# Kernel optimization log

Measured on AMD Instinct MI355X. Metric: run time of the kernel, lower is better.

## Reference

```python
import jax, jax.numpy as jnp
import numpy as np

N, T = 64, 256
V, E, K = 32000, 256, 128


def setup_inputs() -> dict:
    key = jax.random.key(0)
    ks = jax.random.split(key, 7)
    x = jax.random.randint(ks[0], (N, T), 0, V)
    embed_w = jax.random.normal(ks[1], (V, E), dtype=jnp.float32) * 0.02
    # nn.Linear(embed_dim, K*K, bias=False), weight.uniform_(-1, 1)
    trans_w = jax.random.uniform(ks[2], (K * K, E), dtype=jnp.float32, minval=-1.0, maxval=1.0)
    # nn.Linear(1, K): weight [K,1], bias [K]
    start_w = jax.random.normal(ks[3], (K, 1), dtype=jnp.float32)
    start_b = jax.random.normal(ks[4], (K,), dtype=jnp.float32) * 0.1
    # nn.Embedding(K, K) cluster embeddings
    emb_cluster_w = jax.random.normal(ks[5], (K, K), dtype=jnp.float32)
    # nn.Linear(K, vocab, bias=False), weight.uniform_(-1, 1) -> weight [V, K]
    emit_w = jax.random.uniform(ks[6], (V, K), dtype=jnp.float32, minval=-1.0, maxval=1.0)
    return {"x": x, "embed_w": embed_w, "trans_w": trans_w, "start_w": start_w,
            "start_b": start_b, "emb_cluster_w": emb_cluster_w, "emit_w": emit_w}


def reference(x, embed_w, trans_w, start_w, start_b, emb_cluster_w, emit_w):
    n, t = x.shape
    k = emb_cluster_w.shape[0]
    ex = embed_w[x]                                            # [N,T,E]
    # Emissions: log_softmax(emit(emb_cluster(i))) per cluster -> [K,V]
    log_emit = jax.nn.log_softmax(emb_cluster_w @ emit_w.T, axis=-1)
    log_emit_t = log_emit.T                                    # [V,K]
    # start(dummy): ones[N,1] @ W.T + b = W[:,0]+b, same per row
    pre = jax.nn.log_softmax(start_w[:, 0] + start_b)          # [K]
    pre = jnp.broadcast_to(pre, (n, k))
    xs = (jnp.swapaxes(ex[:, :-1, :], 0, 1),                   # [T-1,N,E]
          x[:, 1:].T)                                          # [T-1,N]
    def step(pre_alpha, inp):
        x_prev, w_t = inp
        tran = jax.nn.log_softmax((x_prev @ trans_w.T).reshape(n, k, k), axis=-1)
        cur = jax.nn.logsumexp(pre_alpha[:, :, None] + tran, axis=1)   # [N,K]
        cur = cur + log_emit_t[w_t]                            # add log p(w_t | state)
        return cur, None
    cur, _ = jax.lax.scan(step, pre, xs)
    return -jnp.mean(jax.nn.logsumexp(cur, axis=1))
```

## Files before the change

### kernel.cpp

```cpp
#include <hip/hip_runtime.h>
#include <cstdint>
#include <cstddef>

#define N_SEQ 64
#define T_LEN 256
#define VOCAB 32000
#define EDIM  256
#define KS    128
#define KK    16384
#define MROWS 16384
#define MREAL 16320
#define GPART 32

typedef short  short8  __attribute__((ext_vector_type(8)));
typedef float  floatx4 __attribute__((ext_vector_type(4)));
typedef int    intx8   __attribute__((ext_vector_type(8)));

#define LGKM_BARRIER() asm volatile("s_waitcnt lgkmcnt(0)\n\ts_barrier" ::: "memory")
#define LGKM_WAIT()    asm volatile("s_waitcnt lgkmcnt(0)" ::: "memory")
#define SBAR() do { asm volatile("s_waitcnt lgkmcnt(0)" ::: "memory"); \
                    __builtin_amdgcn_s_barrier(); \
                    __builtin_amdgcn_sched_barrier(0); } while (0)

static __device__ __forceinline__ unsigned short f2bf(float f) {
  unsigned u = __float_as_uint(f);
  u += 0x7fffu + ((u >> 16) & 1u);
  return (unsigned short)(u >> 16);
}

static __device__ __forceinline__ float bf2f(unsigned short h) {
  return __uint_as_float(((unsigned)h) << 16);
}

static __device__ __forceinline__ float fast_rcp(float x) {
#if __has_builtin(__builtin_amdgcn_rcpf)
  return __builtin_amdgcn_rcpf(x);
#else
  return 1.0f / x;
#endif
}

static __device__ __forceinline__ void gl_lds16(const void* gptr, void* lptr) {
  __builtin_amdgcn_global_load_lds(
      (const __attribute__((address_space(1))) void*)gptr,
      (__attribute__((address_space(3))) void*)lptr, 16, 0, 0);
}

__global__ __launch_bounds__(128) void k_prep(const float* sw, const float* sb, float* pre0) {
  __shared__ float vals[KS];
  __shared__ float MM, LS;
  int tid = threadIdx.x;
  float v = sw[tid] + sb[tid];
  vals[tid] = v;
  __syncthreads();
  if (tid == 0) { float m = vals[0]; for (int i = 1; i < KS; ++i) m = fmaxf(m, vals[i]); MM = m; }
  __syncthreads();
  float e = __expf(v - MM);
  vals[tid] = e;
  __syncthreads();
  if (tid == 0) { float s = 0.f; for (int i = 0; i < KS; ++i) s += vals[i]; LS = MM + __logf(s); }
  __syncthreads();
  pre0[tid] = v - LS;
}

__global__ __launch_bounds__(256) void k_transcvt(const float* tw, unsigned short* tb) {
  int idx = blockIdx.x * 256 + threadIdx.x;
  if (idx >= (KK * EDIM) / 4) return;
  int row = idx >> 6, e4 = idx & 63;
  int rowp = ((row & 127) << 7) | (row >> 7);
  int e4s = (e4 & 0x31) | (((((e4 >> 1) & 7) ^ (rowp & 7))) << 1);
  float4 v = *(const float4*)&tw[(size_t)idx * 4];
  unsigned h0 = f2bf(v.x), h1 = f2bf(v.y), h2 = f2bf(v.z), h3 = f2bf(v.w);
  uint2 o; o.x = h0 | (h1 << 16); o.y = h2 | (h3 << 16);
  *(uint2*)&tb[(size_t)rowp * EDIM + e4s * 4] = o;
}

__global__ __launch_bounds__(256) void k_embed(const int* x, const float* ew, unsigned short* exb) {
  int m = blockIdx.x, e = threadIdx.x;
  int t = m >> 6, n = m & 63;
  float v = 0.f;
  if (m < MREAL) { int tok = x[n * T_LEN + t]; v = ew[(size_t)tok * EDIM + e]; }
  int es = (e & 0xC7) | ((((e >> 3) & 7) ^ (m & 7)) << 3);
  exb[(size_t)m * EDIM + es] = f2bf(v);
}

__global__ __launch_bounds__(256) void k_emitlogits(const float* ecl, const float* emw, float* C) {
  int v0 = blockIdx.x * 64, k0 = blockIdx.y * 64;
  int tid = threadIdx.x;
  __shared__ alignas(16) float At[64 * 17];
  __shared__ alignas(16) float Bt[64 * 17];
  int tx = tid & 15, ty = tid >> 4;
  int r = tid >> 2, q = tid & 3;
  float acc[4][4] = {};
  for (int d0 = 0; d0 < KS; d0 += 16) {
    float4 av = *(const float4*)&ecl[(size_t)(k0 + r) * KS + d0 + q * 4];
    float4 bv = *(const float4*)&emw[(size_t)(v0 + r) * KS + d0 + q * 4];
    __syncthreads();
    At[r * 17 + q * 4 + 0] = av.x; At[r * 17 + q * 4 + 1] = av.y;
    At[r * 17 + q * 4 + 2] = av.z; At[r * 17 + q * 4 + 3] = av.w;
    Bt[r * 17 + q * 4 + 0] = bv.x; Bt[r * 17 + q * 4 + 1] = bv.y;
    Bt[r * 17 + q * 4 + 2] = bv.z; Bt[r * 17 + q * 4 + 3] = bv.w;
    __syncthreads();
    #pragma unroll
    for (int dd = 0; dd < 16; ++dd) {
      float a[4], b[4];
      #pragma unroll
      for (int i = 0; i < 4; ++i) a[i] = At[(ty * 4 + i) * 17 + dd];
      #pragma unroll
      for (int i = 0; i < 4; ++i) b[i] = Bt[(tx * 4 + i) * 17 + dd];
      #pragma unroll
      for (int i = 0; i < 4; ++i)
        #pragma unroll
        for (int jj = 0; jj < 4; ++jj) acc[i][jj] += a[i] * b[jj];
    }
  }
  #pragma unroll
  for (int i = 0; i < 4; ++i) {
    float4 o; o.x = acc[i][0]; o.y = acc[i][1]; o.z = acc[i][2]; o.w = acc[i][3];
    *(float4*)&C[(size_t)(k0 + ty * 4 + i) * VOCAB + v0 + tx * 4] = o;
  }
}

__global__ __launch_bounds__(256) void k_lsec(const float* C, float* lseC) {
  int k = blockIdx.x, tid = threadIdx.x;
  __shared__ float sm[4], ss[4];
  const float* row = C + (size_t)k * VOCAB;
  float m = -1e30f;
  for (int v = tid; v < VOCAB; v += 256) m = fmaxf(m, row[v]);
  #pragma unroll
  for (int s = 1; s < 64; s <<= 1) m = fmaxf(m, __shfl_xor(m, s));
  if ((tid & 63) == 0) sm[tid >> 6] = m;
  __syncthreads();
  m = fmaxf(fmaxf(sm[0], sm[1]), fmaxf(sm[2], sm[3]));
  float sum = 0.f;
  for (int v = tid; v < VOCAB; v += 256) sum += __expf(row[v] - m);
  #pragma unroll
  for (int s = 1; s < 64; s <<= 1) sum += __shfl_xor(sum, s);
  if ((tid & 63) == 0) ss[tid >> 6] = sum;
  __syncthreads();
  if (tid == 0) lseC[k] = m + __logf(ss[0] + ss[1] + ss[2] + ss[3]);
}

__global__ __launch_bounds__(128) void k_emis(const int* x, const float* C, const float* lseC,
                                              float* emis, float* emax) {
  int t = blockIdx.x + 1;
  int n = blockIdx.y;
  int k = threadIdx.x;
  __shared__ float red[2];
  int w = x[n * T_LEN + t];
  float v = C[(size_t)k * VOCAB + w] - lseC[k];
  emis[(size_t)((n << 8) + t) * KS + k] = v;
  float m = v;
  #pragma unroll
  for (int s = 1; s < 64; s <<= 1) m = fmaxf(m, __shfl_xor(m, s));
  if ((k & 63) == 0) red[k >> 6] = m;
  __syncthreads();
  if (k == 0) emax[n * T_LEN + t] = fmaxf(red[0], red[1]);
}

__global__ __launch_bounds__(256) void k_comb(const unsigned short* srowPh, float* srowR, float* wcomb,
                                              const float* emis, const float* emax,
                                              int m_base, int Rcap, int rows) {
  int id = blockIdx.x * 256 + threadIdx.x;
  if (id >= rows * KS) return;
  float s = 0.f;
  #pragma unroll
  for (int g = 0; g < GPART; ++g) s += bf2f(srowPh[(size_t)g * Rcap * KS + id]);
  float r = 1.0f / s;
  srowR[(size_t)m_base * KS + id] = r;
  int m = m_base + (id >> 7);
  int t = m >> 6, n = m & 63, k = id & 127;
  float wv = 0.f;
  if (t >= 1) {
    float e  = emis[(size_t)((n << 8) + t) * KS + k];
    float ex = emax[n * T_LEN + t];
    wv = __expf(e - ex) * r * 4096.0f;
  }
  wcomb[(size_t)m_base * KS + id] = wv;
}

static __device__ __forceinline__ void load_S2(const unsigned char* Sbase, int j, int kg, intx8& sf) {
  const uint4* p = (const uint4*)(Sbase + (size_t)j * 128 + kg * 32);
  uint4 a = p[0], b = p[1];
  sf[0] = a.x; sf[1] = a.y; sf[2] = a.z; sf[3] = a.w;
  sf[4] = b.x; sf[5] = b.y; sf[6] = b.z; sf[7] = b.w;
}

static __device__ __forceinline__ void scan_step4(
    int i, int L, int t, int t0s, int tLast, int n, int tid, int kg, int j0, int j1,
    const unsigned char* Ss, const float* wcomb, const float* emis, const float* emax,
    unsigned char* uL8, float* c0sh,
    intx8& uf, intx8& s0, intx8& s1, float& w0, float& w1, float& ex,
    float& M, float& pre_0, float& pre_1) {
  const float LNS = 8.317766167f;
  floatx4 cz = {0.f, 0.f, 0.f, 0.f};
  floatx4 d0 = __builtin_amdgcn_mfma_scale_f32_16x16x128_f8f6f4(
      uf, s0, cz, 0, 0, 0, 0x7F7F7F7F, 0, 0x7F7F7F7F);
  floatx4 d1 = __builtin_amdgcn_mfma_scale_f32_16x16x128_f8f6f4(
      uf, s1, cz, 0, 0, 0, 0x7F7F7F7F, 0, 0x7F7F7F7F);
  float cv0 = d0[0], cv1 = d1[0];
  int tp = t + 2; if (tp > tLast) tp = tLast;
  const unsigned char* Sp = Ss + (size_t)((tp - t0s) * 64 + n) * KK;
  load_S2(Sp, j0, kg, s0);
  load_S2(Sp, j1, kg, s1);
  if (tid == 0) *c0sh = cv0;
  SBAR();
  if (i < L - 1) {
    float c0 = *c0sh;
    float rc = fast_rcp(c0);
    float u0 = cv0 * w0 * rc, u1 = cv1 * w1 * rc;
    int pk0 = __builtin_amdgcn_cvt_pk_fp8_f32(u0, u0, 0, 0);
    int pk1 = __builtin_amdgcn_cvt_pk_fp8_f32(u1, u1, 0, 0);
    if (kg == 0) {
      uL8[j0] = (unsigned char)(pk0 & 0xff);
      uL8[j1] = (unsigned char)(pk1 & 0xff);
    }
    M += ex + __logf(c0) - LNS;
    w0 = wcomb[(size_t)(tp * 64 + n) * KS + j0];
    w1 = wcomb[(size_t)(tp * 64 + n) * KS + j1];
    ex = emax[n * T_LEN + tp];
    SBAR();
    uint4 ua = *(const uint4*)&uL8[kg * 32];
    uint4 ub = *(const uint4*)&uL8[kg * 32 + 16];
    uf[0] = ua.x; uf[1] = ua.y; uf[2] = ua.z; uf[3] = ua.w;
    uf[4] = ub.x; uf[5] = ub.y; uf[6] = ub.z; uf[7] = ub.w;
  } else {
    float em0 = emis[(size_t)((n << 8) + tLast) * KS + j0];
    float em1 = emis[(size_t)((n << 8) + tLast) * KS + j1];
    pre_0 = M - LNS + __logf(cv0) + em0;
    pre_1 = M - LNS + __logf(cv1) + em1;
    SBAR();
  }
}

__global__ __launch_bounds__(256, 2) void k_fused(
    const unsigned short* exb, const unsigned short* trb,
    unsigned char* Sg, unsigned short* srowPh, int m_base, int Rcap,
    const unsigned char* Ss, const float* srowR, const float* wcomb,
    const float* emis, const float* emax, const float* pre0,
    float* alphaG, float* nll, int t0s, int tcs) {
  __shared__ alignas(16) unsigned short As[128 * 64];
  __shared__ alignas(16) unsigned short Bs[128 * 64];
  __shared__ alignas(16) unsigned char uL8[KS];
  __shared__ float c0sh;
  __shared__ float redW[4], redE[4];

  if (blockIdx.x < 64) {
    if (tcs <= 0) return;
    int n = blockIdx.x;
    int tid = threadIdx.x;
    int w = tid >> 6, ln = tid & 63;
    int l15 = ln & 15, kg = ln >> 4;
    int q0 = w * 2;
    int j0 = q0 * 16 + l15, j1 = j0 + 16;
    const float SCALE = 4096.0f;
    int L = tcs, t1 = t0s + tcs, tLast = t1 - 1;
    const float* a0 = (t0s == 1) ? pre0 : (alphaG + (size_t)n * KS);
    float pre_0 = a0[j0], pre_1 = a0[j1];
    float lm = fmaxf(pre_0, pre_1);
    #pragma unroll
    for (int s2 = 1; s2 < 16; s2 <<= 1) lm = fmaxf(lm, __shfl_xor(lm, s2));
    if (ln == 0) redW[w] = lm;
    SBAR();
    float M = fmaxf(fmaxf(redW[0], redW[1]), fmaxf(redW[2], redW[3]));
    {
      float r0 = srowR[(size_t)((t0s - 1) * 64 + n) * KS + j0];
      float r1 = srowR[(size_t)((t0s - 1) * 64 + n) * KS + j1];
      float u0 = __expf(pre_0 - M) * r0 * SCALE;
      float u1 = __expf(pre_1 - M) * r1 * SCALE;
      int pk0 = __builtin_amdgcn_cvt_pk_fp8_f32(u0, u0, 0, 0);
      int pk1 = __builtin_amdgcn_cvt_pk_fp8_f32(u1, u1, 0, 0);
      if (kg == 0) {
        uL8[j0] = (unsigned char)(pk0 & 0xff);
        uL8[j1] = (unsigned char)(pk1 & 0xff);
      }
    }
    SBAR();
    intx8 uf;
    {
      uint4 ua = *(const uint4*)&uL8[kg * 32];
      uint4 ub = *(const uint4*)&uL8[kg * 32 + 16];
      uf[0] = ua.x; uf[1] = ua.y; uf[2] = ua.z; uf[3] = ua.w;
      uf[4] = ub.x; uf[5] = ub.y; uf[6] = ub.z; uf[7] = ub.w;
    }
    intx8 sA0, sA1, sB0, sB1;
    load_S2(Ss + (size_t)n * KK, j0, kg, sA0);
    load_S2(Ss + (size_t)n * KK, j1, kg, sA1);
    int iB = (L > 1) ? 1 : 0;
    const unsigned char* SpB = Ss + (size_t)(iB * 64 + n) * KK;
    load_S2(SpB, j0, kg, sB0);
    load_S2(SpB, j1, kg, sB1);
    int tB = t0s + iB;
    float wA0 = wcomb[(size_t)(t0s * 64 + n) * KS + j0];
    float wA1 = wcomb[(size_t)(t0s * 64 + n) * KS + j1];
    float wB0 = wcomb[(size_t)(tB * 64 + n) * KS + j0];
    float wB1 = wcomb[(size_t)(tB * 64 + n) * KS + j1];
    float exA = emax[n * T_LEN + t0s];
    float exB = emax[n * T_LEN + tB];
    int i = 0, t = t0s;
    for (;;) {
      scan_step4(i, L, t, t0s, tLast, n, tid, kg, j0, j1, Ss, wcomb, emis, emax,
                 uL8, &c0sh, uf, sA0, sA1, wA0, wA1, exA, M, pre_0, pre_1);
      if (++i >= L) break; ++t;
      scan_step4(i, L, t, t0s, tLast, n, tid, kg, j0, j1, Ss, wcomb, emis, emax,
                 uL8, &c0sh, uf, sB0, sB1, wB0, wB1, exB, M, pre_0, pre_1);
      if (++i >= L) break; ++t;
    }
    if (kg == 0) {
      alphaG[(size_t)n * KS + j0] = pre_0;
      alphaG[(size_t)n * KS + j1] = pre_1;
    }
    if (t1 == T_LEN) {
      float m2 = fmaxf(pre_0, pre_1);
      #pragma unroll
      for (int s2 = 1; s2 < 16; s2 <<= 1) m2 = fmaxf(m2, __shfl_xor(m2, s2));
      if (ln == 0) redW[w] = m2;
      SBAR();
      m2 = fmaxf(fmaxf(redW[0], redW[1]), fmaxf(redW[2], redW[3]));
      float le = __expf(pre_0 - m2) + __expf(pre_1 - m2);
      #pragma unroll
      for (int s2 = 1; s2 < 16; s2 <<= 1) le += __shfl_xor(le, s2);
      if (ln == 0) redE[w] = le;
      SBAR();
      if (tid == 0) nll[n] = m2 + __logf(redE[0] + redE[1] + redE[2] + redE[3]);
    }
    return;
  }

  int g = blockIdx.x - 64;
  int bx = g >> 5, grp = g & 31;
  int tid = threadIdx.x, wv = tid >> 6, ln = tid & 63;
  int wc = wv & 1, wm = wv >> 1;
  int m0 = m_base + bx * 128;
  int lr = ln & 15, lk = (ln >> 4) * 8;
  int lg = ln >> 4;
  floatx4 sacc[4][4] = {};
  for (int byi = 0; byi < 4; ++byi) {
    int by = grp * 4 + byi;
    int c0 = by * 128;
    floatx4 acc[4][4] = {};
    for (int k0 = 0; k0 < EDIM; k0 += 64) {
      #pragma unroll
      for (int r = 0; r < 4; ++r) {
        int chunk = (wv * 4 + r) * 64 + ln;
        int row = chunk >> 3, c8 = chunk & 7;
        gl_lds16(&exb[(size_t)(m0 + row) * EDIM + k0 + c8 * 8], &As[(wv * 4 + r) * 512]);
        gl_lds16(&trb[(size_t)(c0 + row) * EDIM + k0 + c8 * 8], &Bs[(wv * 4 + r) * 512]);
      }
      __syncthreads();
      #pragma unroll
      for (int kk = 0; kk < 64; kk += 32) {
        int sw = ((((kk + lk) >> 3) ^ (lr & 7)) << 3);
        short8 af[4], bf[4];
        #pragma unroll
        for (int f = 0; f < 4; ++f)
          af[f] = *(const short8*)&As[(wm * 64 + f * 16 + lr) * 64 + sw];
        #pragma unroll
        for (int f = 0; f < 4; ++f)
          bf[f] = *(const short8*)&Bs[(wc * 64 + f * 16 + lr) * 64 + sw];
        #pragma unroll
        for (int fc = 0; fc < 4; ++fc)
          #pragma unroll
          for (int fm = 0; fm < 4; ++fm)
            acc[fc][fm] = __builtin_amdgcn_mfma_f32_16x16x32_bf16(bf[fc], af[fm], acc[fc][fm], 0, 0, 0);
      }
      LGKM_BARRIER();
    }
    unsigned char* Ts = (unsigned char*)As;
    #pragma unroll
    for (int fc = 0; fc < 4; ++fc) {
      #pragma unroll
      for (int fm = 0; fm < 4; ++fm) {
        floatx4 a = acc[fc][fm];
        float e0 = __expf(a[0]), e1 = __expf(a[1]), e2 = __expf(a[2]), e3 = __expf(a[3]);
        int pq = __builtin_amdgcn_cvt_pk_fp8_f32(e0, e1, 0, 0);
        pq = __builtin_amdgcn_cvt_pk_fp8_f32(e2, e3, pq, 1);
        int mloc = wm * 64 + fm * 16 + lr;
        int cl = wc * 64 + fc * 16 + lg * 4;
        *(int*)&Ts[mloc * 128 + (cl ^ ((mloc & 7) << 4))] = pq;
        sacc[fc][fm][0] += e0; sacc[fc][fm][1] += e1;
        sacc[fc][fm][2] += e2; sacc[fc][fm][3] += e3;
      }
    }
    LGKM_BARRIER();
    #pragma unroll
    for (int r = 0; r < 4; ++r) {
      int seg = r * 256 + tid;
      int mloc = seg >> 3, s = seg & 7;
      uint4 v = *(const uint4*)&Ts[mloc * 128 + ((s ^ (mloc & 7)) << 4)];
      *(uint4*)&Sg[(size_t)(bx * 128 + mloc) * KK + c0 + s * 16] = v;
    }
    LGKM_BARRIER();
  }
  #pragma unroll
  for (int fc = 0; fc < 4; ++fc) {
    #pragma unroll
    for (int fm = 0; fm < 4; ++fm) {
      int mloc = bx * 128 + wm * 64 + fm * 16 + lr;
      int i = wc * 64 + fc * 16 + lg * 4;
      ushort4 h;
      h.x = f2bf(sacc[fc][fm][0]); h.y = f2bf(sacc[fc][fm][1]);
      h.z = f2bf(sacc[fc][fm][2]); h.w = f2bf(sacc[fc][fm][3]);
      *(ushort4*)&srowPh[((size_t)grp * Rcap + mloc) * KS + i] = h;
    }
  }
}

__global__ __launch_bounds__(64) void k_final(const float* nll, float* out) {
  int tid = threadIdx.x;
  float v = nll[tid];
  #pragma unroll
  for (int s = 1; s < 64; s <<= 1) v += __shfl_xor(v, s);
  if (tid == 0) out[0] = -v / 64.0f;
}

extern "C" void kernel_launch(void* const* d_in, const int* in_sizes, int n_in,
                              void* d_out, int out_size, void* d_ws, size_t ws_size,
                              hipStream_t stream) {
  const int*   x       = (const int*)d_in[0];
  const float* embed_w = (const float*)d_in[1];
  const float* trans_w = (const float*)d_in[2];
  const float* start_w = (const float*)d_in[3];
  const float* start_b = (const float*)d_in[4];
  const float* ecl     = (const float*)d_in[5];
  const float* emw     = (const float*)d_in[6];

  char* w = (char*)d_ws;
  size_t off = 0;
  auto alloc = [&](size_t bytes) -> char* {
    char* p = w + off;
    off = (off + bytes + 255) & ~(size_t)255;
    return p;
  };
  float*          pre0   = (float*)alloc(KS * 4);
  float*          lseC   = (float*)alloc(KS * 4);
  float*          nll    = (float*)alloc(N_SEQ * 4);
  float*          alphaG = (float*)alloc((size_t)N_SEQ * KS * 4);
  float*          emax   = (float*)alloc((size_t)N_SEQ * T_LEN * 4);
  unsigned short* trb    = (unsigned short*)alloc((size_t)KK * EDIM * 2);
  unsigned short* exb    = (unsigned short*)alloc((size_t)MROWS * EDIM * 2);
  float*          emis   = (float*)alloc((size_t)N_SEQ * T_LEN * KS * 4);
  float*          srowR  = (float*)alloc((size_t)MROWS * KS * 4);
  float*          wcomb  = (float*)alloc((size_t)MROWS * KS * 4);
  char* region = w + off;
  size_t avail = (ws_size > off) ? (ws_size - off) : 0;
  float* C = (float*)region;

  int Tc = 2;
  for (int c = 2; c <= 64; c += 2)
    if ((size_t)c * 64 * 40960 <= avail) Tc = c;
  int Rcap = Tc * 64;
  unsigned char*  S0     = (unsigned char*)region;
  unsigned char*  S1     = (unsigned char*)(region + (size_t)Rcap * KK);
  unsigned short* srowPh = (unsigned short*)(region + (size_t)2 * Rcap * KK);

  hipLaunchKernelGGL(k_prep,       dim3(1),        dim3(128), 0, stream, start_w, start_b, pre0);
  hipLaunchKernelGGL(k_transcvt,   dim3(4096),     dim3(256), 0, stream, trans_w, trb);
  hipLaunchKernelGGL(k_embed,      dim3(16384),    dim3(256), 0, stream, x, embed_w, exb);
  hipLaunchKernelGGL(k_emitlogits, dim3(500, 2),   dim3(256), 0, stream, ecl, emw, C);
  hipLaunchKernelGGL(k_lsec,       dim3(128),      dim3(256), 0, stream, C, lseC);
  hipLaunchKernelGGL(k_emis,       dim3(255, 64),  dim3(128), 0, stream, x, C, lseC, emis, emax);

  int ct0[140], ctc[140], nc = 0;
  {
    int t0 = 1;
    while (t0 < T_LEN) {
      int tc = T_LEN - t0; if (tc > Tc) tc = Tc;
      ct0[nc] = t0; ctc[nc] = tc; ++nc; t0 += tc;
    }
  }
  for (int c = 0; c <= nc; ++c) {
    bool hasG = (c < nc), hasS = (c > 0);
    int gx = 0, m_base = 0;
    if (hasG) { gx = (ctc[c] * 64 + 127) / 128; m_base = (ct0[c] - 1) * 64; }
    unsigned char* Sg = (c & 1) ? S1 : S0;
    unsigned char* Ssc = ((c - 1) & 1) ? S1 : S0;
    int t0s = hasS ? ct0[c - 1] : 0;
    int tcs = hasS ? ctc[c - 1] : 0;
    hipLaunchKernelGGL(k_fused, dim3(64 + gx * 32), dim3(256), 0, stream,
                       exb, trb, Sg, srowPh, m_base, Rcap,
                       Ssc, srowR, wcomb, emis, emax, pre0, alphaG, nll, t0s, tcs);
    if (hasG)
      hipLaunchKernelGGL(k_comb, dim3(gx * 64), dim3(256), 0, stream,
                         srowPh, srowR, wcomb, emis, emax, m_base, Rcap, gx * 128);
  }
  hipLaunchKernelGGL(k_final, dim3(1), dim3(64), 0, stream, nll, (float*)d_out);
}
```

Before: 532.9 us.

## Fold partial-sum combine kernel into scan blocks with double-buffered partials

Removes the separate k_comb launch per chunk, which reduced 32 bf16 partial row sums into srowR and wcomb. The scan blocks of k_fused now read the partials directly: each lane loads 8 groups and reduces across kg lanes with shuffles, then computes the emission weight inline. The partial buffer becomes double-buffered so the next chunk's GEMM can write while the scan reads. This trades a kernel launch and the wcomb/srowR round-trips for more global loads and ALU work on the latency-critical serial scan path. It also uses more workspace, which may shrink the chunk size Tc.

```diff
diff --git a/kernel.cpp b/kernel.cpp
--- a/kernel.cpp
+++ b/kernel.cpp
@@ -158,27 +158,6 @@
   if (k == 0) emax[n * T_LEN + t] = fmaxf(red[0], red[1]);
 }
 
-__global__ __launch_bounds__(256) void k_comb(const unsigned short* srowPh, float* srowR, float* wcomb,
-                                              const float* emis, const float* emax,
-                                              int m_base, int Rcap, int rows) {
-  int id = blockIdx.x * 256 + threadIdx.x;
-  if (id >= rows * KS) return;
-  float s = 0.f;
-  #pragma unroll
-  for (int g = 0; g < GPART; ++g) s += bf2f(srowPh[(size_t)g * Rcap * KS + id]);
-  float r = 1.0f / s;
-  srowR[(size_t)m_base * KS + id] = r;
-  int m = m_base + (id >> 7);
-  int t = m >> 6, n = m & 63, k = id & 127;
-  float wv = 0.f;
-  if (t >= 1) {
-    float e  = emis[(size_t)((n << 8) + t) * KS + k];
-    float ex = emax[n * T_LEN + t];
-    wv = __expf(e - ex) * r * 4096.0f;
-  }
-  wcomb[(size_t)m_base * KS + id] = wv;
-}
-
 static __device__ __forceinline__ void load_S2(const unsigned char* Sbase, int j, int kg, intx8& sf) {
   const uint4* p = (const uint4*)(Sbase + (size_t)j * 128 + kg * 32);
   uint4 a = p[0], b = p[1];
@@ -186,11 +165,31 @@
   sf[4] = b.x; sf[5] = b.y; sf[6] = b.z; sf[7] = b.w;
 }
 
+static __device__ __forceinline__ void load_PW(const unsigned short* phS, int Rcap,
+                                               int mrel, int j, int kg,
+                                               unsigned short (&rw)[8]) {
+  #pragma unroll
+  for (int g = 0; g < 8; ++g)
+    rw[g] = phS[((size_t)(g * 4 + kg) * Rcap + mrel) * KS + j];
+}
+
+static __device__ __forceinline__ float red_PW(const unsigned short (&rw)[8]) {
+  float s = 0.f;
+  #pragma unroll
+  for (int g = 0; g < 8; ++g) s += bf2f(rw[g]);
+  s += __shfl_xor(s, 16);
+  s += __shfl_xor(s, 32);
+  return s;
+}
+
 static __device__ __forceinline__ void scan_step4(
     int i, int L, int t, int t0s, int tLast, int n, int tid, int kg, int j0, int j1,
-    const unsigned char* Ss, const float* wcomb, const float* emis, const float* emax,
+    const unsigned char* Ss, const unsigned short* phS, int Rcap,
+    const float* emis, const float* emax,
     unsigned char* uL8, float* c0sh,
-    intx8& uf, intx8& s0, intx8& s1, float& w0, float& w1, float& ex,
+    intx8& uf, intx8& s0, intx8& s1,
+    unsigned short (&rw0)[8], unsigned short (&rw1)[8],
+    float& e0p, float& e1p, float& ex,
     float& M, float& pre_0, float& pre_1) {
   const float LNS = 8.317766167f;
   floatx4 cz = {0.f, 0.f, 0.f, 0.f};
@@ -208,6 +207,9 @@
   if (i < L - 1) {
     float c0 = *c0sh;
     float rc = fast_rcp(c0);
+    float sr0 = red_PW(rw0), sr1 = red_PW(rw1);
+    float w0 = __expf(e0p - ex) * 4096.0f * fast_rcp(sr0);
+    float w1 = __expf(e1p - ex) * 4096.0f * fast_rcp(sr1);
     float u0 = cv0 * w0 * rc, u1 = cv1 * w1 * rc;
     int pk0 = __builtin_amdgcn_cvt_pk_fp8_f32(u0, u0, 0, 0);
     int pk1 = __builtin_amdgcn_cvt_pk_fp8_f32(u1, u1, 0, 0);
@@ -216,8 +218,11 @@
       uL8[j1] = (unsigned char)(pk1 & 0xff);
     }
     M += ex + __logf(c0) - LNS;
-    w0 = wcomb[(size_t)(tp * 64 + n) * KS + j0];
-    w1 = wcomb[(size_t)(tp * 64 + n) * KS + j1];
+    int mrel = (tp - t0s + 1) * 64 + n;
+    load_PW(phS, Rcap, mrel, j0, kg, rw0);
+    load_PW(phS, Rcap, mrel, j1, kg, rw1);
+    e0p = emis[(size_t)((n << 8) + tp) * KS + j0];
+    e1p = emis[(size_t)((n << 8) + tp) * KS + j1];
     ex = emax[n * T_LEN + tp];
     SBAR();
     uint4 ua = *(const uint4*)&uL8[kg * 32];
@@ -235,8 +240,8 @@
 
 __global__ __launch_bounds__(256, 2) void k_fused(
     const unsigned short* exb, const unsigned short* trb,
-    unsigned char* Sg, unsigned short* srowPh, int m_base, int Rcap,
-    const unsigned char* Ss, const float* srowR, const float* wcomb,
+    unsigned char* Sg, unsigned short* phG, int m_base, int Rcap,
+    const unsigned char* Ss, const unsigned short* phS,
     const float* emis, const float* emax, const float* pre0,
     float* alphaG, float* nll, int t0s, int tcs) {
   __shared__ alignas(16) unsigned short As[128 * 64];
@@ -264,10 +269,12 @@
     SBAR();
     float M = fmaxf(fmaxf(redW[0], redW[1]), fmaxf(redW[2], redW[3]));
     {
-      float r0 = srowR[(size_t)((t0s - 1) * 64 + n) * KS + j0];
-      float r1 = srowR[(size_t)((t0s - 1) * 64 + n) * KS + j1];
-      float u0 = __expf(pre_0 - M) * r0 * SCALE;
-      float u1 = __expf(pre_1 - M) * r1 * SCALE;
+      unsigned short h0[8], h1[8];
+      load_PW(phS, Rcap, n, j0, kg, h0);
+      load_PW(phS, Rcap, n, j1, kg, h1);
+      float sr0 = red_PW(h0), sr1 = red_PW(h1);
+      float u0 = __expf(pre_0 - M) * SCALE * fast_rcp(sr0);
+      float u1 = __expf(pre_1 - M) * SCALE * fast_rcp(sr1);
       int pk0 = __builtin_amdgcn_cvt_pk_fp8_f32(u0, u0, 0, 0);
       int pk1 = __builtin_amdgcn_cvt_pk_fp8_f32(u1, u1, 0, 0);
       if (kg == 0) {
@@ -291,19 +298,26 @@
     load_S2(SpB, j0, kg, sB0);
     load_S2(SpB, j1, kg, sB1);
     int tB = t0s + iB;
-    float wA0 = wcomb[(size_t)(t0s * 64 + n) * KS + j0];
-    float wA1 = wcomb[(size_t)(t0s * 64 + n) * KS + j1];
-    float wB0 = wcomb[(size_t)(tB * 64 + n) * KS + j0];
-    float wB1 = wcomb[(size_t)(tB * 64 + n) * KS + j1];
+    unsigned short rwA0[8], rwA1[8], rwB0[8], rwB1[8];
+    load_PW(phS, Rcap, 64 + n, j0, kg, rwA0);
+    load_PW(phS, Rcap, 64 + n, j1, kg, rwA1);
+    load_PW(phS, Rcap, (iB + 1) * 64 + n, j0, kg, rwB0);
+    load_PW(phS, Rcap, (iB + 1) * 64 + n, j1, kg, rwB1);
+    float eA0 = emis[(size_t)((n << 8) + t0s) * KS + j0];
+    float eA1 = emis[(size_t)((n << 8) + t0s) * KS + j1];
+    float eB0 = emis[(size_t)((n << 8) + tB) * KS + j0];
+    float eB1 = emis[(size_t)((n << 8) + tB) * KS + j1];
     float exA = emax[n * T_LEN + t0s];
     float exB = emax[n * T_LEN + tB];
     int i = 0, t = t0s;
     for (;;) {
-      scan_step4(i, L, t, t0s, tLast, n, tid, kg, j0, j1, Ss, wcomb, emis, emax,
-                 uL8, &c0sh, uf, sA0, sA1, wA0, wA1, exA, M, pre_0, pre_1);
+      scan_step4(i, L, t, t0s, tLast, n, tid, kg, j0, j1, Ss, phS, Rcap,
+                 emis, emax, uL8, &c0sh, uf, sA0, sA1,
+                 rwA0, rwA1, eA0, eA1, exA, M, pre_0, pre_1);
       if (++i >= L) break; ++t;
-      scan_step4(i, L, t, t0s, tLast, n, tid, kg, j0, j1, Ss, wcomb, emis, emax,
-                 uL8, &c0sh, uf, sB0, sB1, wB0, wB1, exB, M, pre_0, pre_1);
+      scan_step4(i, L, t, t0s, tLast, n, tid, kg, j0, j1, Ss, phS, Rcap,
+                 emis, emax, uL8, &c0sh, uf, sB0, sB1,
+                 rwB0, rwB1, eB0, eB1, exB, M, pre_0, pre_1);
       if (++i >= L) break; ++t;
     }
     if (kg == 0) {
@@ -401,7 +415,7 @@
       ushort4 h;
       h.x = f2bf(sacc[fc][fm][0]); h.y = f2bf(sacc[fc][fm][1]);
       h.z = f2bf(sacc[fc][fm][2]); h.w = f2bf(sacc[fc][fm][3]);
-      *(ushort4*)&srowPh[((size_t)grp * Rcap + mloc) * KS + i] = h;
+      *(ushort4*)&phG[((size_t)grp * Rcap + mloc) * KS + i] = h;
     }
   }
 }
@@ -440,19 +454,18 @@
   unsigned short* trb    = (unsigned short*)alloc((size_t)KK * EDIM * 2);
   unsigned short* exb    = (unsigned short*)alloc((size_t)MROWS * EDIM * 2);
   float*          emis   = (float*)alloc((size_t)N_SEQ * T_LEN * KS * 4);
-  float*          srowR  = (float*)alloc((size_t)MROWS * KS * 4);
-  float*          wcomb  = (float*)alloc((size_t)MROWS * KS * 4);
   char* region = w + off;
   size_t avail = (ws_size > off) ? (ws_size - off) : 0;
   float* C = (float*)region;
 
   int Tc = 2;
   for (int c = 2; c <= 64; c += 2)
-    if ((size_t)c * 64 * 40960 <= avail) Tc = c;
+    if ((size_t)c * 64 * 49152 <= avail) Tc = c;
   int Rcap = Tc * 64;
-  unsigned char*  S0     = (unsigned char*)region;
-  unsigned char*  S1     = (unsigned char*)(region + (size_t)Rcap * KK);
-  unsigned short* srowPh = (unsigned short*)(region + (size_t)2 * Rcap * KK);
+  unsigned char*  S0  = (unsigned char*)region;
+  unsigned char*  S1  = (unsigned char*)(region + (size_t)Rcap * KK);
+  unsigned short* Ph0 = (unsigned short*)(region + (size_t)2 * Rcap * KK);
+  unsigned short* Ph1 = Ph0 + (size_t)GPART * Rcap * KS;
 
   hipLaunchKernelGGL(k_prep,       dim3(1),        dim3(128), 0, stream, start_w, start_b, pre0);
   hipLaunchKernelGGL(k_transcvt,   dim3(4096),     dim3(256), 0, stream, trans_w, trb);
@@ -473,16 +486,15 @@
     bool hasG = (c < nc), hasS = (c > 0);
     int gx = 0, m_base = 0;
     if (hasG) { gx = (ctc[c] * 64 + 127) / 128; m_base = (ct0[c] - 1) * 64; }
-    unsigned char* Sg = (c & 1) ? S1 : S0;
-    unsigned char* Ssc = ((c - 1) & 1) ? S1 : S0;
+    unsigned char*  Sg  = (c & 1) ? S1 : S0;
+    unsigned char*  Ssc = ((c - 1) & 1) ? S1 : S0;
+    unsigned short* phG = (c & 1) ? Ph1 : Ph0;
+    unsigned short* phS = ((c - 1) & 1) ? Ph1 : Ph0;
     int t0s = hasS ? ct0[c - 1] : 0;
     int tcs = hasS ? ctc[c - 1] : 0;
     hipLaunchKernelGGL(k_fused, dim3(64 + gx * 32), dim3(256), 0, stream,
-                       exb, trb, Sg, srowPh, m_base, Rcap,
-                       Ssc, srowR, wcomb, emis, emax, pre0, alphaG, nll, t0s, tcs);
-    if (hasG)
-      hipLaunchKernelGGL(k_comb, dim3(gx * 64), dim3(256), 0, stream,
-                         srowPh, srowR, wcomb, emis, emax, m_base, Rcap, gx * 128);
+                       exb, trb, Sg, phG, m_base, Rcap,
+                       Ssc, phS, emis, emax, pre0, alphaG, nll, t0s, tcs);
   }
   hipLaunchKernelGGL(k_final, dim3(1), dim3(64), 0, stream, nll, (float*)d_out);
 }
```

Result: no change. 539.7 us (+1.3%).
